# Optimization experiments

Measured on AMD Instinct MI355X. Metric: run time of the kernel, lower is better.

## Reference

```python
import jax, jax.numpy as jnp
import numpy as np

N, M, D = 8192, 8192, 1024

def setup_inputs() -> dict:
    key = jax.random.key(0)
    k1, k2 = jax.random.split(key)
    encoder_outputs = jax.random.normal(k1, (N, D), dtype=jnp.float32)
    fact_emb = jax.random.normal(k2, (M, D), dtype=jnp.float32)
    return {"encoder_outputs": encoder_outputs, "fact_emb": fact_emb}

def reference(encoder_outputs, fact_emb):
    # energy: [N, M] = encoder_outputs @ fact_emb^T (unscaled)
    energy = jnp.einsum('nd,md->nm', encoder_outputs, fact_emb)
    weights = jax.nn.softmax(energy, axis=1)          # softmax over facts
    outputs = jnp.einsum('nm,md->nd', weights, fact_emb)
    return (outputs, weights)
```

## Files before the change

kernel.cpp:

```cpp
#include <hip/hip_runtime.h>
#include <hip/hip_bf16.h>
#include <math.h>
#include <stdint.h>

#define N_ROWS 8192
#define M_FACTS 8192
#define D_DIM 1024

typedef __bf16 bf16x8_t __attribute__((ext_vector_type(8)));
typedef __bf16 bf16x4_t __attribute__((ext_vector_type(4)));
typedef float f32x4_t __attribute__((ext_vector_type(4)));

#define BM 128
#define BN 128
#define BK 32
#define PADK 40

__device__ __forceinline__ void gload_lds16(const void* g, void* lds) {
  __builtin_amdgcn_global_load_lds(
      (__attribute__((address_space(1))) void*)(uintptr_t)g,
      (__attribute__((address_space(3))) void*)(uint32_t)(uintptr_t)lds,
      16, 0, 0);
}


__global__ __launch_bounds__(256) void split_hi_lo(const float* __restrict__ X,
                                                   __bf16* __restrict__ H,
                                                   __bf16* __restrict__ L) {
  int i = blockIdx.x * 256 + threadIdx.x;
  float4 v = ((const float4*)X)[i];
  float f[4] = {v.x, v.y, v.z, v.w};
  bf16x4_t h, l;
#pragma unroll
  for (int q = 0; q < 4; q++) {
    __bf16 hh = (__bf16)f[q];
    h[q] = hh;
    l[q] = (__bf16)(f[q] - (float)hh);
  }
  ((bf16x4_t*)H)[i] = h;
  ((bf16x4_t*)L)[i] = l;
}

__global__ __launch_bounds__(256) void split_concat_E(const float* __restrict__ X,
                                                      __bf16* __restrict__ A2) {
  int idx = blockIdx.x * 256 + threadIdx.x;
  int n = idx >> 8, d4 = idx & 255;
  float4 v = ((const float4*)X)[idx];
  float f[4] = {v.x, v.y, v.z, v.w};
  bf16x4_t h, l;
#pragma unroll
  for (int q = 0; q < 4; q++) {
    __bf16 hh = (__bf16)f[q];
    h[q] = hh;
    l[q] = (__bf16)(f[q] - (float)hh);
  }
  size_t base = (size_t)n * 3072 + d4 * 4;
  *(bf16x4_t*)(A2 + base) = h;
  *(bf16x4_t*)(A2 + base + 1024) = l;
  *(bf16x4_t*)(A2 + base + 2048) = h;
}

__global__ __launch_bounds__(256) void split_concat_F(const float* __restrict__ X,
                                                      __bf16* __restrict__ B2) {
  int idx = blockIdx.x * 256 + threadIdx.x;
  int m = idx >> 8, d4 = idx & 255;
  float4 v = ((const float4*)X)[idx];
  float f[4] = {v.x, v.y, v.z, v.w};
  bf16x4_t h, l;
#pragma unroll
  for (int q = 0; q < 4; q++) {
    __bf16 hh = (__bf16)f[q];
    h[q] = hh;
    l[q] = (__bf16)(f[q] - (float)hh);
  }
  size_t base = (size_t)m * 3072 + d4 * 4;
  *(bf16x4_t*)(B2 + base) = h;
  *(bf16x4_t*)(B2 + base + 1024) = h;
  *(bf16x4_t*)(B2 + base + 2048) = l;
}

__global__ __launch_bounds__(256) void transpose_f_bf16(const float* __restrict__ F,
                                                        __bf16* __restrict__ Ft) {
  __shared__ float t[64 * 69];
  const int tid = threadIdx.x;
  const int m0 = blockIdx.x * 64, d0 = blockIdx.y * 64;
#pragma unroll
  for (int p = 0; p < 4; p++) {
    int flat = p * 256 + tid;
    int m = flat >> 4, dq = flat & 15;
    float4 v = *(const float4*)(F + (size_t)(m0 + m) * D_DIM + d0 + dq * 4);
    t[(dq * 4 + 0) * 69 + m] = v.x;
    t[(dq * 4 + 1) * 69 + m] = v.y;
    t[(dq * 4 + 2) * 69 + m] = v.z;
    t[(dq * 4 + 3) * 69 + m] = v.w;
  }
  __syncthreads();
#pragma unroll
  for (int q = 0; q < 2; q++) {
    int id = q * 256 + tid;
    int d = id >> 3, c = id & 7;
    const float* row = t + d * 69 + c * 8;
    bf16x8_t o;
#pragma unroll
    for (int i = 0; i < 8; i++) o[i] = (__bf16)row[i];
    *(bf16x8_t*)(Ft + (size_t)(d0 + d) * M_FACTS + m0 + c * 8) = o;
  }
}

template <int RH>
__global__ __launch_bounds__(512, 2) void gemm_big(const __bf16* __restrict__ A,
                                                   const __bf16* __restrict__ B,
                                                   float* __restrict__ C,
                                                   int K, int lda, int ldb, int ldc) {
  constexpr int BMT = RH * 128;
  __shared__ __align__(16) __bf16 sA[2][BMT * 64];
  __shared__ __align__(16) __bf16 sB[2][256 * 64];
  const int tid = threadIdx.x;
  const int wave = tid >> 6, lane = tid & 63;
  const int wm = wave >> 2;
  const int wn = wave & 3;
  const int lrow = lane & 15, quad = lane >> 4;
  const int row0 = blockIdx.x * BMT;
  const int col0 = blockIdx.y * 256;

  auto STAGE = [&](int buf, int kt) {
    const int ko = kt * 64;
#pragma unroll
    for (int k = 0; k < RH * 2; k++) {
      int g = tid + 512 * k;
      int sr = g >> 3;
      int so = ((g & 7) ^ (sr & 7)) << 3;
      gload_lds16(A + (size_t)(row0 + sr) * lda + ko + so, &sA[buf][g * 8]);
    }
#pragma unroll
    for (int k = 0; k < 4; k++) {
      int g = tid + 512 * k;
      int sr = g >> 3;
      int so = ((g & 7) ^ (sr & 7)) << 3;
      gload_lds16(B + (size_t)(col0 + sr) * ldb + ko + so, &sB[buf][g * 8]);
    }
  };

  f32x4_t acc[RH * 4][4];
#pragma unroll
  for (int i = 0; i < RH * 4; i++)
#pragma unroll
    for (int j = 0; j < 4; j++) acc[i][j] = (f32x4_t){0.f, 0.f, 0.f, 0.f};

  const int nkt = K >> 6;

  STAGE(0, 0);
  asm volatile("s_waitcnt vmcnt(0)" ::: "memory");
  __builtin_amdgcn_s_barrier();
  __builtin_amdgcn_sched_barrier(0);

  for (int t = 0; t < nkt; ++t) {
    const int cur = t & 1;
    const __bf16* lA = &sA[cur][0];
    const __bf16* lB = &sB[cur][0];

    if (t + 1 < nkt) STAGE(cur ^ 1, t + 1);
    __builtin_amdgcn_sched_barrier(0);

    bf16x8_t bfr[4][2];
#pragma unroll
    for (int cf = 0; cf < 4; ++cf) {
      const int c = wn * 64 + cf * 16 + lrow;
#pragma unroll
      for (int ks = 0; ks < 2; ++ks)
        bfr[cf][ks] = *(const bf16x8_t*)(lB + c * 64 + (((ks * 4 + quad) ^ (c & 7)) << 3));
    }
#pragma unroll
    for (int rh = 0; rh < RH; ++rh) {
      bf16x8_t af[4][2];
#pragma unroll
      for (int rf = 0; rf < 4; ++rf) {
        const int r = wm * (RH * 64) + rh * 64 + rf * 16 + lrow;
#pragma unroll
        for (int ks = 0; ks < 2; ++ks)
          af[rf][ks] = *(const bf16x8_t*)(lA + r * 64 + (((ks * 4 + quad) ^ (r & 7)) << 3));
      }
      __builtin_amdgcn_s_setprio(1);
#pragma unroll
      for (int rf = 0; rf < 4; ++rf)
#pragma unroll
        for (int cf = 0; cf < 4; ++cf)
#pragma unroll
          for (int ks = 0; ks < 2; ++ks)
            acc[rh * 4 + rf][cf] = __builtin_amdgcn_mfma_f32_16x16x32_bf16(
                af[rf][ks], bfr[cf][ks], acc[rh * 4 + rf][cf], 0, 0, 0);
      __builtin_amdgcn_s_setprio(0);
    }

    __builtin_amdgcn_sched_barrier(0);
    if (t + 1 < nkt) {
      asm volatile("s_waitcnt vmcnt(0)" ::: "memory");
      __builtin_amdgcn_s_barrier();
      __builtin_amdgcn_sched_barrier(0);
    }
  }

#pragma unroll
  for (int i = 0; i < RH * 4; ++i) {
    const int rbase = row0 + wm * (RH * 64) + (i >> 2) * 64 + (i & 3) * 16 + quad * 4;
#pragma unroll
    for (int j = 0; j < 4; ++j) {
      const int c = col0 + wn * 64 + j * 16 + lrow;
#pragma unroll
      for (int r = 0; r < 4; ++r) C[(size_t)(rbase + r) * ldc + c] = acc[i][j][r];
    }
  }
}

__global__ __launch_bounds__(256) void gemm1_fast(const __bf16* __restrict__ Eh,
                                                  const __bf16* __restrict__ El,
                                                  const __bf16* __restrict__ Fh,
                                                  const __bf16* __restrict__ Fl,
                                                  float* __restrict__ C,
                                                  int row_base) {
  __shared__ __bf16 sAh[BM * BK], sAl[BM * BK], sBh[BN * BK], sBl[BN * BK];
  const int tid = threadIdx.x;
  const int wave = tid >> 6, lane = tid & 63;
  const int row0 = row_base + blockIdx.x * BM, col0 = blockIdx.y * BN;
  const int wm = wave >> 1, wn = wave & 1;
  const int lrow = lane & 15, quad = lane >> 4;

  f32x4_t acc[4][4];
#pragma unroll
  for (int i = 0; i < 4; i++)
#pragma unroll
    for (int j = 0; j < 4; j++) acc[i][j] = (f32x4_t){0.f, 0.f, 0.f, 0.f};

  for (int k0 = 0; k0 < D_DIM; k0 += BK) {
#pragma unroll
    for (int r = 0; r < 2; r++) {
      int c = (r * 4 + wave) * 64 + lane;
      int row = c >> 2;
      int ko = (c & 3) << 3;
      size_t ga = (size_t)(row0 + row) * D_DIM + k0 + ko;
      size_t gb = (size_t)(col0 + row) * D_DIM + k0 + ko;
      gload_lds16(Eh + ga, sAh + c * 8);
      gload_lds16(El + ga, sAl + c * 8);
      gload_lds16(Fh + gb, sBh + c * 8);
      gload_lds16(Fl + gb, sBl + c * 8);
    }
    __syncthreads();

    bf16x8_t ah[4], al[4], bh[4], bl[4];
#pragma unroll
    for (int i = 0; i < 4; i++) {
      int ra = (wm * 64 + i * 16 + lrow) * BK + quad * 8;
      ah[i] = *(const bf16x8_t*)(sAh + ra);
      al[i] = *(const bf16x8_t*)(sAl + ra);
      int rb = (wn * 64 + i * 16 + lrow) * BK + quad * 8;
      bh[i] = *(const bf16x8_t*)(sBh + rb);
      bl[i] = *(const bf16x8_t*)(sBl + rb);
    }
#pragma unroll
    for (int i = 0; i < 4; i++)
#pragma unroll
      for (int j = 0; j < 4; j++) {
        acc[i][j] = __builtin_amdgcn_mfma_f32_16x16x32_bf16(ah[i], bh[j], acc[i][j], 0, 0, 0);
        acc[i][j] = __builtin_amdgcn_mfma_f32_16x16x32_bf16(ah[i], bl[j], acc[i][j], 0, 0, 0);
        acc[i][j] = __builtin_amdgcn_mfma_f32_16x16x32_bf16(al[i], bh[j], acc[i][j], 0, 0, 0);
      }
    __syncthreads();
  }

#pragma unroll
  for (int i = 0; i < 4; i++) {
    int rbase = row0 + wm * 64 + i * 16 + quad * 4;
#pragma unroll
    for (int j = 0; j < 4; j++) {
      int c = col0 + wn * 64 + j * 16 + lrow;
#pragma unroll
      for (int r = 0; r < 4; r++) C[(size_t)(rbase + r) * M_FACTS + c] = acc[i][j][r];
    }
  }
}

__global__ __launch_bounds__(256) void gemm2_reg(const __bf16* __restrict__ Wb,
                                                 const __bf16* __restrict__ Ft,
                                                 float* __restrict__ O,
                                                 int out_row0) {
  __shared__ __bf16 sW[2][BM * BK];
  __shared__ __bf16 sF[2][BN * BK];
  const int tid = threadIdx.x;
  const int wave = tid >> 6, lane = tid & 63;
  const int row0 = blockIdx.x * BM;
  const int col0 = blockIdx.y * BN;
  const int wm = wave >> 1, wn = wave & 1;
  const int lrow = lane & 15, quad = lane >> 4;

  const int id0 = wave * 64 + lane;
  const int r0 = id0 >> 2, c0 = (id0 & 3) << 3;
  const int id1 = id0 + 256;
  const int r1 = id1 >> 2, c1 = (id1 & 3) << 3;

  const __bf16* gW = Wb + (size_t)row0 * M_FACTS;
  const __bf16* gF = Ft + (size_t)col0 * M_FACTS;

  f32x4_t acc[4][4];
#pragma unroll
  for (int i = 0; i < 4; i++)
#pragma unroll
    for (int j = 0; j < 4; j++) acc[i][j] = (f32x4_t){0.f, 0.f, 0.f, 0.f};

  bf16x8_t rW0, rW1, rF0, rF1;
  rW0 = *(const bf16x8_t*)(gW + (size_t)r0 * M_FACTS + c0);
  rW1 = *(const bf16x8_t*)(gW + (size_t)r1 * M_FACTS + c1);
  rF0 = *(const bf16x8_t*)(gF + (size_t)r0 * M_FACTS + c0);
  rF1 = *(const bf16x8_t*)(gF + (size_t)r1 * M_FACTS + c1);
  *(bf16x8_t*)(&sW[0][id0 * 8]) = rW0;
  *(bf16x8_t*)(&sW[0][id1 * 8]) = rW1;
  *(bf16x8_t*)(&sF[0][id0 * 8]) = rF0;
  *(bf16x8_t*)(&sF[0][id1 * 8]) = rF1;
  rW0 = *(const bf16x8_t*)(gW + (size_t)r0 * M_FACTS + BK + c0);
  rW1 = *(const bf16x8_t*)(gW + (size_t)r1 * M_FACTS + BK + c1);
  rF0 = *(const bf16x8_t*)(gF + (size_t)r0 * M_FACTS + BK + c0);
  rF1 = *(const bf16x8_t*)(gF + (size_t)r1 * M_FACTS + BK + c1);
  __syncthreads();

  const int NT = M_FACTS / BK;
  for (int it = 0; it < NT; it++) {
    const int cur = it & 1;
    bf16x8_t a[4], b[4];
#pragma unroll
    for (int i = 0; i < 4; i++) {
      a[i] = *(const bf16x8_t*)(&sW[cur][(wm * 64 + i * 16 + lrow) * BK + quad * 8]);
      b[i] = *(const bf16x8_t*)(&sF[cur][(wn * 64 + i * 16 + lrow) * BK + quad * 8]);
    }
#pragma unroll
    for (int i = 0; i < 4; i++)
#pragma unroll
      for (int j = 0; j < 4; j++)
        acc[i][j] = __builtin_amdgcn_mfma_f32_16x16x32_bf16(a[i], b[j], acc[i][j], 0, 0, 0);

    __syncthreads();
    if (it + 1 < NT) {
      const int nxt = cur ^ 1;
      *(bf16x8_t*)(&sW[nxt][id0 * 8]) = rW0;
      *(bf16x8_t*)(&sW[nxt][id1 * 8]) = rW1;
      *(bf16x8_t*)(&sF[nxt][id0 * 8]) = rF0;
      *(bf16x8_t*)(&sF[nxt][id1 * 8]) = rF1;
      if (it + 2 < NT) {
        const int ko = (it + 2) * BK;
        rW0 = *(const bf16x8_t*)(gW + (size_t)r0 * M_FACTS + ko + c0);
        rW1 = *(const bf16x8_t*)(gW + (size_t)r1 * M_FACTS + ko + c1);
        rF0 = *(const bf16x8_t*)(gF + (size_t)r0 * M_FACTS + ko + c0);
        rF1 = *(const bf16x8_t*)(gF + (size_t)r1 * M_FACTS + ko + c1);
      }
      __syncthreads();
    }
  }

#pragma unroll
  for (int i = 0; i < 4; i++) {
    int rbase = out_row0 + row0 + wm * 64 + i * 16 + quad * 4;
#pragma unroll
    for (int j = 0; j < 4; j++) {
      int c = col0 + wn * 64 + j * 16 + lrow;
#pragma unroll
      for (int r = 0; r < 4; r++) O[(size_t)(rbase + r) * D_DIM + c] = acc[i][j][r];
    }
  }
}

__global__ __launch_bounds__(256) void gemm2_mid(const float* __restrict__ W,
                                                 const __bf16* __restrict__ Ft,
                                                 float* __restrict__ O) {
  __shared__ __bf16 sW[BM * BK], sF[BN * BK];
  const int tid = threadIdx.x;
  const int wave = tid >> 6, lane = tid & 63;
  const int row0 = blockIdx.x * BM, col0 = blockIdx.y * BN;
  const int wm = wave >> 1, wn = wave & 1;
  const int lrow = lane & 15, quad = lane >> 4;

  f32x4_t acc[4][4];
#pragma unroll
  for (int i = 0; i < 4; i++)
#pragma unroll
    for (int j = 0; j < 4; j++) acc[i][j] = (f32x4_t){0.f, 0.f, 0.f, 0.f};

  for (int k0 = 0; k0 < M_FACTS; k0 += BK) {
#pragma unroll
    for (int r = 0; r < 2; r++) {
      int c = (r * 4 + wave) * 64 + lane;
      int row = c >> 2;
      int ko = (c & 3) << 3;
      gload_lds16(Ft + (size_t)(col0 + row) * M_FACTS + k0 + ko, sF + c * 8);
    }
#pragma unroll
    for (int it = 0; it < 4; it++) {
      int flat = it * 256 + tid;
      int r = flat >> 3, q = flat & 7;
      float4 v = *(const float4*)(W + (size_t)(row0 + r) * M_FACTS + k0 + q * 4);
      bf16x4_t h;
      h[0] = (__bf16)v.x;
      h[1] = (__bf16)v.y;
      h[2] = (__bf16)v.z;
      h[3] = (__bf16)v.w;
      *(bf16x4_t*)(sW + r * BK + q * 4) = h;
    }
    __syncthreads();

    bf16x8_t a[4], b[4];
#pragma unroll
    for (int i = 0; i < 4; i++) {
      a[i] = *(const bf16x8_t*)(sW + (wm * 64 + i * 16 + lrow) * BK + quad * 8);
      b[i] = *(const bf16x8_t*)(sF + (wn * 64 + i * 16 + lrow) * BK + quad * 8);
    }
#pragma unroll
    for (int i = 0; i < 4; i++)
#pragma unroll
      for (int j = 0; j < 4; j++)
        acc[i][j] = __builtin_amdgcn_mfma_f32_16x16x32_bf16(a[i], b[j], acc[i][j], 0, 0, 0);
    __syncthreads();
  }

#pragma unroll
  for (int i = 0; i < 4; i++) {
    int rbase = row0 + wm * 64 + i * 16 + quad * 4;
#pragma unroll
    for (int j = 0; j < 4; j++) {
      int c = col0 + wn * 64 + j * 16 + lrow;
#pragma unroll
      for (int r = 0; r < 4; r++) O[(size_t)(rbase + r) * D_DIM + c] = acc[i][j][r];
    }
  }
}

template <bool EMIT_BF16>
__global__ __launch_bounds__(256) void softmax_rows_t(float* __restrict__ W,
                                                      __bf16* __restrict__ Wb) {
  __shared__ float red[8];
  const int tid = threadIdx.x;
  float* p = W + (size_t)blockIdx.x * M_FACTS;

  float4 v[8];
  float mx = -3.4e38f;
#pragma unroll
  for (int i = 0; i < 8; i++) {
    v[i] = *(const float4*)(p + (size_t)(i * 256 + tid) * 4);
    mx = fmaxf(mx, fmaxf(fmaxf(v[i].x, v[i].y), fmaxf(v[i].z, v[i].w)));
  }
#pragma unroll
  for (int off = 32; off >= 1; off >>= 1) mx = fmaxf(mx, __shfl_xor(mx, off));
  const int wave = tid >> 6, lane = tid & 63;
  if (lane == 0) red[wave] = mx;
  __syncthreads();
  mx = fmaxf(fmaxf(red[0], red[1]), fmaxf(red[2], red[3]));

  float s = 0.f;
#pragma unroll
  for (int i = 0; i < 8; i++) {
    v[i].x = __expf(v[i].x - mx);
    v[i].y = __expf(v[i].y - mx);
    v[i].z = __expf(v[i].z - mx);
    v[i].w = __expf(v[i].w - mx);
    s += v[i].x + v[i].y + v[i].z + v[i].w;
  }
#pragma unroll
  for (int off = 32; off >= 1; off >>= 1) s += __shfl_xor(s, off);
  if (lane == 0) red[4 + wave] = s;
  __syncthreads();
  s = red[4] + red[5] + red[6] + red[7];
  float inv = 1.0f / s;
  __bf16* pb = EMIT_BF16 ? (Wb + (size_t)blockIdx.x * M_FACTS) : nullptr;
#pragma unroll
  for (int i = 0; i < 8; i++) {
    v[i].x *= inv;
    v[i].y *= inv;
    v[i].z *= inv;
    v[i].w *= inv;
    *(float4*)(p + (size_t)(i * 256 + tid) * 4) = v[i];
    if (EMIT_BF16) {
      bf16x4_t h;
      h[0] = (__bf16)v[i].x;
      h[1] = (__bf16)v[i].y;
      h[2] = (__bf16)v[i].z;
      h[3] = (__bf16)v[i].w;
      *(bf16x4_t*)(pb + (size_t)(i * 256 + tid) * 4) = h;
    }
  }
}

__global__ __launch_bounds__(256) void gemm1_energy(const float* __restrict__ A,
                                                    const float* __restrict__ B,
                                                    float* __restrict__ C) {
  __shared__ __align__(16) __bf16 sAh[BM * PADK];
  __shared__ __align__(16) __bf16 sAl[BM * PADK];
  __shared__ __align__(16) __bf16 sBh[BN * PADK];
  __shared__ __align__(16) __bf16 sBl[BN * PADK];

  const int tid = threadIdx.x;
  const int row0 = blockIdx.x * BM, col0 = blockIdx.y * BN;
  const int wave = tid >> 6, lane = tid & 63;
  const int wm = wave >> 1, wn = wave & 1;
  const int lrow = lane & 15, quad = lane >> 4;

  f32x4_t acc[4][4];
#pragma unroll
  for (int i = 0; i < 4; i++)
#pragma unroll
    for (int j = 0; j < 4; j++) acc[i][j] = (f32x4_t){0.f, 0.f, 0.f, 0.f};

  for (int k0 = 0; k0 < D_DIM; k0 += BK) {
    __syncthreads();
#pragma unroll
    for (int it = 0; it < 4; it++) {
      int flat = it * 256 + tid;
      int r = flat >> 3, kq = flat & 7;
      float4 va = *(const float4*)(A + (size_t)(row0 + r) * D_DIM + k0 + kq * 4);
      float4 vb = *(const float4*)(B + (size_t)(col0 + r) * D_DIM + k0 + kq * 4);
      float fa[4] = {va.x, va.y, va.z, va.w};
      float fb[4] = {vb.x, vb.y, vb.z, vb.w};
      bf16x4_t ah, al, bh, bl;
#pragma unroll
      for (int q = 0; q < 4; q++) {
        __bf16 h = (__bf16)fa[q];
        ah[q] = h;
        al[q] = (__bf16)(fa[q] - (float)h);
        __bf16 g = (__bf16)fb[q];
        bh[q] = g;
        bl[q] = (__bf16)(fb[q] - (float)g);
      }
      *(bf16x4_t*)(sAh + r * PADK + kq * 4) = ah;
      *(bf16x4_t*)(sAl + r * PADK + kq * 4) = al;
      *(bf16x4_t*)(sBh + r * PADK + kq * 4) = bh;
      *(bf16x4_t*)(sBl + r * PADK + kq * 4) = bl;
    }
    __syncthreads();

    bf16x8_t a_h[4], a_l[4], b_h[4], b_l[4];
#pragma unroll
    for (int i = 0; i < 4; i++) {
      int ra = wm * 64 + i * 16 + lrow;
      a_h[i] = *(const bf16x8_t*)(sAh + ra * PADK + quad * 8);
      a_l[i] = *(const bf16x8_t*)(sAl + ra * PADK + quad * 8);
      int rb = wn * 64 + i * 16 + lrow;
      b_h[i] = *(const bf16x8_t*)(sBh + rb * PADK + quad * 8);
      b_l[i] = *(const bf16x8_t*)(sBl + rb * PADK + quad * 8);
    }
#pragma unroll
    for (int i = 0; i < 4; i++)
#pragma unroll
      for (int j = 0; j < 4; j++) {
        acc[i][j] = __builtin_amdgcn_mfma_f32_16x16x32_bf16(a_h[i], b_h[j], acc[i][j], 0, 0, 0);
        acc[i][j] = __builtin_amdgcn_mfma_f32_16x16x32_bf16(a_h[i], b_l[j], acc[i][j], 0, 0, 0);
        acc[i][j] = __builtin_amdgcn_mfma_f32_16x16x32_bf16(a_l[i], b_h[j], acc[i][j], 0, 0, 0);
      }
  }

#pragma unroll
  for (int i = 0; i < 4; i++) {
    int rbase = row0 + wm * 64 + i * 16 + quad * 4;
#pragma unroll
    for (int j = 0; j < 4; j++) {
      int c = col0 + wn * 64 + j * 16 + lrow;
#pragma unroll
      for (int r = 0; r < 4; r++) C[(size_t)(rbase + r) * M_FACTS + c] = acc[i][j][r];
    }
  }
}

__global__ __launch_bounds__(256) void gemm2_out(const float* __restrict__ W,
                                                 const float* __restrict__ F,
                                                 float* __restrict__ O) {
  __shared__ __align__(16) __bf16 sW[BM * PADK];
  __shared__ __align__(16) __bf16 sFt[BN * PADK];

  const int tid = threadIdx.x;
  const int row0 = blockIdx.x * BM, col0 = blockIdx.y * BN;
  const int wave = tid >> 6, lane = tid & 63;
  const int wm = wave >> 1, wn = wave & 1;
  const int lrow = lane & 15, quad = lane >> 4;

  f32x4_t acc[4][4];
#pragma unroll
  for (int i = 0; i < 4; i++)
#pragma unroll
    for (int j = 0; j < 4; j++) acc[i][j] = (f32x4_t){0.f, 0.f, 0.f, 0.f};

  for (int k0 = 0; k0 < M_FACTS; k0 += BK) {
    __syncthreads();
#pragma unroll
    for (int it = 0; it < 4; it++) {
      int flat = it * 256 + tid;
      int r = flat >> 3, kq = flat & 7;
      float4 v = *(const float4*)(W + (size_t)(row0 + r) * M_FACTS + k0 + kq * 4);
      bf16x4_t h;
      h[0] = (__bf16)v.x;
      h[1] = (__bf16)v.y;
      h[2] = (__bf16)v.z;
      h[3] = (__bf16)v.w;
      *(bf16x4_t*)(sW + r * PADK + kq * 4) = h;
    }
#pragma unroll
    for (int it = 0; it < 4; it++) {
      int flat = it * 256 + tid;
      int m = flat >> 5, dq = flat & 31;
      float4 v = *(const float4*)(F + (size_t)(k0 + m) * D_DIM + col0 + dq * 4);
      sFt[(dq * 4 + 0) * PADK + m] = (__bf16)v.x;
      sFt[(dq * 4 + 1) * PADK + m] = (__bf16)v.y;
      sFt[(dq * 4 + 2) * PADK + m] = (__bf16)v.z;
      sFt[(dq * 4 + 3) * PADK + m] = (__bf16)v.w;
    }
    __syncthreads();

    bf16x8_t a[4], b[4];
#pragma unroll
    for (int i = 0; i < 4; i++) {
      a[i] = *(const bf16x8_t*)(sW + (wm * 64 + i * 16 + lrow) * PADK + quad * 8);
      b[i] = *(const bf16x8_t*)(sFt + (wn * 64 + i * 16 + lrow) * PADK + quad * 8);
    }
#pragma unroll
    for (int i = 0; i < 4; i++)
#pragma unroll
      for (int j = 0; j < 4; j++)
        acc[i][j] = __builtin_amdgcn_mfma_f32_16x16x32_bf16(a[i], b[j], acc[i][j], 0, 0, 0);
  }

#pragma unroll
  for (int i = 0; i < 4; i++) {
    int rbase = row0 + wm * 64 + i * 16 + quad * 4;
#pragma unroll
    for (int j = 0; j < 4; j++) {
      int c = col0 + wn * 64 + j * 16 + lrow;
#pragma unroll
      for (int r = 0; r < 4; r++) O[(size_t)(rbase + r) * D_DIM + c] = acc[i][j][r];
    }
  }
}

extern "C" void kernel_launch(void* const* d_in, const int* in_sizes, int n_in,
                              void* d_out, int out_size, void* d_ws, size_t ws_size,
                              hipStream_t stream) {
  const float* E = (const float*)d_in[0];
  const float* F = (const float*)d_in[1];
  float* outputs = (float*)d_out;
  float* weights = (float*)d_out + (size_t)N_ROWS * D_DIM;

  const size_t MB = 1ull << 20;
  char* ws = (char*)d_ws;

  const bool t1 = ws_size >= 144 * MB;
  const bool t2 = !t1 && ws_size >= 80 * MB;
  const bool hasFtOnly = !t1 && !t2 && ws_size >= 16 * MB;

  if (t1) {
    __bf16* Ft = (__bf16*)(ws + 0 * MB);
    __bf16* A2 = (__bf16*)(ws + 16 * MB);
    __bf16* B2 = (__bf16*)(ws + 64 * MB);
    __bf16* Wb = (__bf16*)(ws + 16 * MB);

    transpose_f_bf16<<<dim3(M_FACTS / 64, D_DIM / 64), 256, 0, stream>>>(F, Ft);
    split_concat_E<<<dim3((N_ROWS * D_DIM) / 1024), 256, 0, stream>>>(E, A2);
    split_concat_F<<<dim3((M_FACTS * D_DIM) / 1024), 256, 0, stream>>>(F, B2);

    gemm_big<2><<<dim3(N_ROWS / 256, M_FACTS / 256), 512, 0, stream>>>(
        A2, B2, weights, 3072, 3072, 3072, M_FACTS);

    softmax_rows_t<true><<<dim3(N_ROWS), 256, 0, stream>>>(weights, Wb);

    gemm_big<1><<<dim3(N_ROWS / 128, D_DIM / 256), 512, 0, stream>>>(
        Wb, Ft, outputs, M_FACTS, M_FACTS, M_FACTS, D_DIM);
  } else if (t2) {
    __bf16* Ft = (__bf16*)(ws + 0 * MB);
    __bf16* Eh = (__bf16*)(ws + 16 * MB);
    __bf16* El = (__bf16*)(ws + 32 * MB);
    __bf16* Fh = (__bf16*)(ws + 48 * MB);
    __bf16* Fl = (__bf16*)(ws + 64 * MB);
    __bf16* Wb = (__bf16*)(ws + 16 * MB);

    transpose_f_bf16<<<dim3(M_FACTS / 64, D_DIM / 64), 256, 0, stream>>>(F, Ft);
    split_hi_lo<<<dim3((N_ROWS * D_DIM) / 1024), 256, 0, stream>>>(E, Eh, El);
    split_hi_lo<<<dim3((M_FACTS * D_DIM) / 1024), 256, 0, stream>>>(F, Fh, Fl);
    gemm1_fast<<<dim3(N_ROWS / BM, M_FACTS / BN), 256, 0, stream>>>(Eh, El, Fh, Fl,
                                                                    weights, 0);
    const int HALF = N_ROWS / 2;
    for (int h = 0; h < 2; h++) {
      float* Wchunk = weights + (size_t)h * HALF * M_FACTS;
      softmax_rows_t<true><<<dim3(HALF), 256, 0, stream>>>(Wchunk, Wb);
      gemm2_reg<<<dim3(HALF / BM, D_DIM / BN), 256, 0, stream>>>(Wb, Ft, outputs, h * HALF);
    }
  } else {
    __bf16* Ft = (__bf16*)ws;
    if (hasFtOnly) {
      transpose_f_bf16<<<dim3(M_FACTS / 64, D_DIM / 64), 256, 0, stream>>>(F, Ft);
    }
    gemm1_energy<<<dim3(N_ROWS / BM, M_FACTS / BN), 256, 0, stream>>>(E, F, weights);
    softmax_rows_t<false><<<dim3(N_ROWS), 256, 0, stream>>>(weights, nullptr);
    if (hasFtOnly) {
      gemm2_mid<<<dim3(N_ROWS / BM, D_DIM / BN), 256, 0, stream>>>(weights, Ft, outputs);
    } else {
      gemm2_out<<<dim3(N_ROWS / BM, D_DIM / BN), 256, 0, stream>>>(weights, F, outputs);
    }
  }
}
```

Measured before the change: 944.5 us.

## Split GEMM k-step into two phases interleaving prefetch with MFMA compute

Replaces the templated GEMM with a phased version that splits each k-tile into two halves. Each half loads its A fragments from LDS, issues half of the next tile's global-to-LDS prefetch, then runs MFMAs, so memory issue is interleaved with compute rather than front-loaded. The second GEMM's tiling also changes from 128x256 to 256x128 output tiles, and the column tile size is now a template parameter. This adds extra barriers per iteration and changes LDS footprint and occupancy for the second GEMM.

```diff
diff --git a/kernel.cpp b/kernel.cpp
--- a/kernel.cpp
+++ b/kernel.cpp
@@ -107,33 +107,33 @@
   }
 }
 
-template <int RH>
-__global__ __launch_bounds__(512, 2) void gemm_big(const __bf16* __restrict__ A,
-                                                   const __bf16* __restrict__ B,
-                                                   float* __restrict__ C,
-                                                   int K, int lda, int ldb, int ldc) {
-  constexpr int BMT = RH * 128;
-  __shared__ __align__(16) __bf16 sA[2][BMT * 64];
-  __shared__ __align__(16) __bf16 sB[2][256 * 64];
+template <int CH>
+__global__ __launch_bounds__(512, 2) void gemm_ph(const __bf16* __restrict__ A,
+                                                  const __bf16* __restrict__ B,
+                                                  float* __restrict__ C,
+                                                  int K, int lda, int ldb, int ldc) {
+  constexpr int BNT = CH * 64;
+  __shared__ __align__(16) __bf16 sA[2][256 * 64];
+  __shared__ __align__(16) __bf16 sB[2][BNT * 64];
   const int tid = threadIdx.x;
   const int wave = tid >> 6, lane = tid & 63;
   const int wm = wave >> 2;
   const int wn = wave & 3;
   const int lrow = lane & 15, quad = lane >> 4;
-  const int row0 = blockIdx.x * BMT;
-  const int col0 = blockIdx.y * 256;
-
-  auto STAGE = [&](int buf, int kt) {
+  const int row0 = blockIdx.x * 256;
+  const int col0 = blockIdx.y * BNT;
+
+  auto STAGE = [&](int buf, int kt, int half) {
     const int ko = kt * 64;
 #pragma unroll
-    for (int k = 0; k < RH * 2; k++) {
+    for (int k = half * 2; k < half * 2 + 2; k++) {
       int g = tid + 512 * k;
       int sr = g >> 3;
       int so = ((g & 7) ^ (sr & 7)) << 3;
       gload_lds16(A + (size_t)(row0 + sr) * lda + ko + so, &sA[buf][g * 8]);
     }
 #pragma unroll
-    for (int k = 0; k < 4; k++) {
+    for (int k = half * (CH / 2); k < (half + 1) * (CH / 2); k++) {
       int g = tid + 512 * k;
       int sr = g >> 3;
       int so = ((g & 7) ^ (sr & 7)) << 3;
@@ -141,15 +141,16 @@
     }
   };
 
-  f32x4_t acc[RH * 4][4];
-#pragma unroll
-  for (int i = 0; i < RH * 4; i++)
-#pragma unroll
-    for (int j = 0; j < 4; j++) acc[i][j] = (f32x4_t){0.f, 0.f, 0.f, 0.f};
+  f32x4_t acc[8][CH];
+#pragma unroll
+  for (int i = 0; i < 8; i++)
+#pragma unroll
+    for (int j = 0; j < CH; j++) acc[i][j] = (f32x4_t){0.f, 0.f, 0.f, 0.f};
 
   const int nkt = K >> 6;
 
-  STAGE(0, 0);
+  STAGE(0, 0, 0);
+  STAGE(0, 0, 1);
   asm volatile("s_waitcnt vmcnt(0)" ::: "memory");
   __builtin_amdgcn_s_barrier();
   __builtin_amdgcn_sched_barrier(0);
@@ -158,42 +159,64 @@
     const int cur = t & 1;
     const __bf16* lA = &sA[cur][0];
     const __bf16* lB = &sB[cur][0];
-
-    if (t + 1 < nkt) STAGE(cur ^ 1, t + 1);
-    __builtin_amdgcn_sched_barrier(0);
-
-    bf16x8_t bfr[4][2];
-#pragma unroll
-    for (int cf = 0; cf < 4; ++cf) {
-      const int c = wn * 64 + cf * 16 + lrow;
+    const bool pf = (t + 1 < nkt);
+
+    bf16x8_t bfr[CH][2];
+#pragma unroll
+    for (int cf = 0; cf < CH; ++cf) {
+      const int c = wn * (CH * 16) + cf * 16 + lrow;
 #pragma unroll
       for (int ks = 0; ks < 2; ++ks)
         bfr[cf][ks] = *(const bf16x8_t*)(lB + c * 64 + (((ks * 4 + quad) ^ (c & 7)) << 3));
     }
-#pragma unroll
-    for (int rh = 0; rh < RH; ++rh) {
-      bf16x8_t af[4][2];
-#pragma unroll
-      for (int rf = 0; rf < 4; ++rf) {
-        const int r = wm * (RH * 64) + rh * 64 + rf * 16 + lrow;
+    bf16x8_t af[4][2];
+#pragma unroll
+    for (int rf = 0; rf < 4; ++rf) {
+      const int r = wm * 128 + rf * 16 + lrow;
+#pragma unroll
+      for (int ks = 0; ks < 2; ++ks)
+        af[rf][ks] = *(const bf16x8_t*)(lA + r * 64 + (((ks * 4 + quad) ^ (r & 7)) << 3));
+    }
+    if (pf) STAGE(cur ^ 1, t + 1, 0);
+    __builtin_amdgcn_s_barrier();
+    asm volatile("s_waitcnt lgkmcnt(0)" ::: "memory");
+    __builtin_amdgcn_sched_barrier(0);
+    __builtin_amdgcn_s_setprio(1);
+#pragma unroll
+    for (int rf = 0; rf < 4; ++rf)
+#pragma unroll
+      for (int cf = 0; cf < CH; ++cf)
 #pragma unroll
         for (int ks = 0; ks < 2; ++ks)
-          af[rf][ks] = *(const bf16x8_t*)(lA + r * 64 + (((ks * 4 + quad) ^ (r & 7)) << 3));
-      }
-      __builtin_amdgcn_s_setprio(1);
-#pragma unroll
-      for (int rf = 0; rf < 4; ++rf)
-#pragma unroll
-        for (int cf = 0; cf < 4; ++cf)
-#pragma unroll
-          for (int ks = 0; ks < 2; ++ks)
-            acc[rh * 4 + rf][cf] = __builtin_amdgcn_mfma_f32_16x16x32_bf16(
-                af[rf][ks], bfr[cf][ks], acc[rh * 4 + rf][cf], 0, 0, 0);
-      __builtin_amdgcn_s_setprio(0);
-    }
-
+          acc[rf][cf] = __builtin_amdgcn_mfma_f32_16x16x32_bf16(af[rf][ks], bfr[cf][ks],
+                                                                acc[rf][cf], 0, 0, 0);
+    __builtin_amdgcn_s_setprio(0);
+
+    bf16x8_t ag[4][2];
+#pragma unroll
+    for (int rf = 0; rf < 4; ++rf) {
+      const int r = wm * 128 + 64 + rf * 16 + lrow;
+#pragma unroll
+      for (int ks = 0; ks < 2; ++ks)
+        ag[rf][ks] = *(const bf16x8_t*)(lA + r * 64 + (((ks * 4 + quad) ^ (r & 7)) << 3));
+    }
+    if (pf) STAGE(cur ^ 1, t + 1, 1);
+    __builtin_amdgcn_s_barrier();
+    asm volatile("s_waitcnt lgkmcnt(0)" ::: "memory");
     __builtin_amdgcn_sched_barrier(0);
-    if (t + 1 < nkt) {
+    __builtin_amdgcn_s_setprio(1);
+#pragma unroll
+    for (int rf = 0; rf < 4; ++rf)
+#pragma unroll
+      for (int cf = 0; cf < CH; ++cf)
+#pragma unroll
+        for (int ks = 0; ks < 2; ++ks)
+          acc[4 + rf][cf] = __builtin_amdgcn_mfma_f32_16x16x32_bf16(ag[rf][ks], bfr[cf][ks],
+                                                                    acc[4 + rf][cf], 0, 0, 0);
+    __builtin_amdgcn_s_setprio(0);
+
+    __builtin_amdgcn_sched_barrier(0);
+    if (pf) {
       asm volatile("s_waitcnt vmcnt(0)" ::: "memory");
       __builtin_amdgcn_s_barrier();
       __builtin_amdgcn_sched_barrier(0);
@@ -201,11 +224,11 @@
   }
 
 #pragma unroll
-  for (int i = 0; i < RH * 4; ++i) {
-    const int rbase = row0 + wm * (RH * 64) + (i >> 2) * 64 + (i & 3) * 16 + quad * 4;
-#pragma unroll
-    for (int j = 0; j < 4; ++j) {
-      const int c = col0 + wn * 64 + j * 16 + lrow;
+  for (int i = 0; i < 8; ++i) {
+    const int rbase = row0 + wm * 128 + (i >> 2) * 64 + (i & 3) * 16 + quad * 4;
+#pragma unroll
+    for (int j = 0; j < CH; ++j) {
+      const int c = col0 + wn * (CH * 16) + j * 16 + lrow;
 #pragma unroll
       for (int r = 0; r < 4; ++r) C[(size_t)(rbase + r) * ldc + c] = acc[i][j][r];
     }
@@ -658,12 +681,12 @@
     split_concat_E<<<dim3((N_ROWS * D_DIM) / 1024), 256, 0, stream>>>(E, A2);
     split_concat_F<<<dim3((M_FACTS * D_DIM) / 1024), 256, 0, stream>>>(F, B2);
 
-    gemm_big<2><<<dim3(N_ROWS / 256, M_FACTS / 256), 512, 0, stream>>>(
+    gemm_ph<4><<<dim3(N_ROWS / 256, M_FACTS / 256), 512, 0, stream>>>(
         A2, B2, weights, 3072, 3072, 3072, M_FACTS);
 
     softmax_rows_t<true><<<dim3(N_ROWS), 256, 0, stream>>>(weights, Wb);
 
-    gemm_big<1><<<dim3(N_ROWS / 128, D_DIM / 256), 512, 0, stream>>>(
+    gemm_ph<2><<<dim3(N_ROWS / 256, D_DIM / 128), 512, 0, stream>>>(
         Wb, Ft, outputs, M_FACTS, M_FACTS, M_FACTS, D_DIM);
   } else if (t2) {
     __bf16* Ft = (__bf16*)(ws + 0 * MB);
```

New measurement: 965.3 us. 2.2% more time.
